# Kernel tuning notes

Hardware: AMD Instinct MI355X
Metric: run time of the kernel (lower is better)

The kernel has to match this reference:

```python
import jax, jax.numpy as jnp
import numpy as np

B, P1, P2 = 64, 15, 14            # batch, H/patch+1, W/patch
E0, E1, E2 = 8, 8, 8               # embed_dim per mode (512 total)
H1, H2, H3 = 2, 2, 2               # heads per mode (8 heads total)
X, Y, Z = E0 // H1, E1 // H2, E2 // H3  # per-head dims (4,4,4) -> head_dim 64
SCALE = (X * Y * Z) ** -0.5


def tle(x, W0, W1, W2, b):
    # mode-n products on last three modes (ignore_modes=(0,1,2)) + bias
    y = jnp.einsum('bpqxyz,ax->bpqayz', x, W0)
    y = jnp.einsum('bpqayz,cy->bpqacz', y, W1)
    y = jnp.einsum('bpqacz,dz->bpqacd', y, W2)
    return y + b


def split_heads(t):
    b, p, q = t.shape[:3]
    t = t.reshape(b, p, q, X, H1, Y, H2, Z, H3)
    return t.transpose(0, 1, 2, 4, 6, 8, 3, 5, 7)


def attention_core(x, Wq0, Wq1, Wq2, bq, Wk0, Wk1, Wk2, bk,
                   Wv0, Wv1, Wv2, bv, Wo0, Wo1, Wo2, bo):
    Q = split_heads(tle(x, Wq0, Wq1, Wq2, bq))
    K = split_heads(tle(x, Wk0, Wk1, Wk2, bk))
    V = split_heads(tle(x, Wv0, Wv1, Wv2, bv))
    # scores over spatial patch pairs per (h1,h2,h3) head triple
    attn = jnp.einsum('bpqdefxyz,bmndefxyz->bdefpqmn', Q, K) * SCALE
    b, d, e, f, p, q, m, n = attn.shape
    a = jax.nn.softmax(attn.reshape(b, d, e, f, p, q, m * n), axis=-1)
    a = a.reshape(b, d, e, f, p, q, m, n)
    o = jnp.einsum('bdefpqmn,bmndefxyz->bdefpqxyz', a, V)
    # b h1 h2 h3 p q x y z -> b p q (x h1)(y h2)(z h3)
    o = o.transpose(0, 4, 5, 6, 1, 7, 2, 8, 3).reshape(b, p, q, E0, E1, E2)
    return tle(o, Wo0, Wo1, Wo2, bo)


def setup_inputs() -> dict:
    key = jax.random.key(0)
    ks = jax.random.split(key, 17)
    inp = {'x': jax.random.normal(ks[0], (B, P1, P2, E0, E1, E2), jnp.float32)}
    i = 1
    for name in ('q', 'k', 'v', 'o'):
        for mode, dim in enumerate((E0, E1, E2)):
            inp[f'W{name}{mode}'] = jax.random.normal(ks[i], (dim, dim), jnp.float32) * 0.1
            i += 1
        inp[f'b{name}'] = jax.random.normal(ks[i], (E0, E1, E2), jnp.float32) * 0.02
        i += 1
    return inp


def reference(x, Wq0, Wq1, Wq2, bq, Wk0, Wk1, Wk2, bk,
              Wv0, Wv1, Wv2, bv, Wo0, Wo1, Wo2, bo):
    return attention_core(x, Wq0, Wq1, Wq2, bq, Wk0, Wk1, Wk2, bk,
                          Wv0, Wv1, Wv2, bv, Wo0, Wo1, Wo2, bo)
```

## Files before the change

### kernel.cpp

```cpp
#include <hip/hip_runtime.h>

typedef unsigned int   u32;
typedef unsigned short u16;
typedef float f32x16 __attribute__((ext_vector_type(16)));
typedef short s16x8  __attribute__((ext_vector_type(8)));
typedef u32   u32x4  __attribute__((ext_vector_type(4)));
typedef u32   u32x2  __attribute__((ext_vector_type(2)));

#define B_   64
#define P1_  15
#define P2_  14
#define S_   210
#define SP_  224
#define NT_  (B_*S_)
#define E_   512
#define NH_  8
#define HD_  64
#define KSC  0.18033688011112042f

__device__ __forceinline__ u16 f2bf(float f) {
    u32 u = __float_as_uint(f);
    u += 0x7fffu + ((u >> 16) & 1u);
    return (u16)(u >> 16);
}
__device__ __forceinline__ float bf2f(u16 h) {
    return __uint_as_float(((u32)h) << 16);
}

__device__ __forceinline__ void wfence() {
    asm volatile("s_waitcnt lgkmcnt(0)" ::: "memory");
}

__device__ __forceinline__ void mode_proj(
        const float* xs, float* t1, float* t2,
        const float* __restrict__ W0, const float* __restrict__ W1,
        const float* __restrict__ W2, const float* __restrict__ bb,
        int t, float* y3)
{
    {
        float xv[8];
        #pragma unroll
        for (int i = 0; i < 8; ++i) xv[i] = xs[i*66 + t];
        #pragma unroll
        for (int a = 0; a < 8; ++a) {
            float acc = 0.f;
            #pragma unroll
            for (int i = 0; i < 8; ++i) acc = fmaf(W0[a*8+i], xv[i], acc);
            t1[a*68 + t] = acc;
        }
    }
    wfence();
    {
        const int a = t >> 3, z = t & 7;
        float yv[8];
        #pragma unroll
        for (int y = 0; y < 8; ++y) yv[y] = t1[a*68 + y*8 + z];
        #pragma unroll
        for (int c = 0; c < 8; ++c) {
            float acc = 0.f;
            #pragma unroll
            for (int y = 0; y < 8; ++y) acc = fmaf(W1[c*8+y], yv[y], acc);
            t2[(a*8 + c)*9 + z] = acc;
        }
    }
    wfence();
    {
        float zv[8];
        #pragma unroll
        for (int z = 0; z < 8; ++z) zv[z] = t2[t*9 + z];
        #pragma unroll
        for (int d = 0; d < 8; ++d) {
            float acc = bb[t*8 + d];
            #pragma unroll
            for (int z = 0; z < 8; ++z) acc = fmaf(W2[d*8+z], zv[z], acc);
            y3[d] = acc;
        }
    }
    wfence();
}

__global__ __launch_bounds__(256) void k_qkv(
    const float* __restrict__ x,
    const float* __restrict__ Wq0, const float* __restrict__ Wq1,
    const float* __restrict__ Wq2, const float* __restrict__ bq,
    const float* __restrict__ Wk0, const float* __restrict__ Wk1,
    const float* __restrict__ Wk2, const float* __restrict__ bk,
    const float* __restrict__ Wv0, const float* __restrict__ Wv1,
    const float* __restrict__ Wv2, const float* __restrict__ bv,
    u16* __restrict__ Qo, u16* __restrict__ Ko, u16* __restrict__ Vo)
{
    __shared__ float xs[4][528];
    __shared__ float t1[4][544];
    __shared__ float t2[4][576];
    const int w = threadIdx.x >> 6, t = threadIdx.x & 63;
    const int tok = blockIdx.x*4 + w;
    const int b   = tok / S_;
    const int s   = tok - b * S_;

    const float* xp = x + (size_t)tok * E_;
    #pragma unroll
    for (int k4 = 0; k4 < 2; ++k4) {
        const float4 vv = *reinterpret_cast<const float4*>(xp + k4*256 + t*4);
        const int m0 = k4*4 + (t >> 4);
        const int in = (t*4) & 63;
        xs[w][m0*66 + in + 0] = vv.x;
        xs[w][m0*66 + in + 1] = vv.y;
        xs[w][m0*66 + in + 2] = vv.z;
        xs[w][m0*66 + in + 3] = vv.w;
    }
    wfence();

    const int a  = t >> 3, c = t & 7;
    const int x_ = a >> 1, h1 = a & 1;
    const int y_ = c >> 1, h2 = c & 1;

    float y3[8];

    mode_proj(xs[w], t1[w], t2[w], Wq0, Wq1, Wq2, bq, t, y3);
    #pragma unroll
    for (int h3 = 0; h3 < 2; ++h3) {
        const int h = (((h1 << 1) | h2) << 1) | h3;
        ushort4 v;
        v.x = f2bf(y3[0 + h3]); v.y = f2bf(y3[2 + h3]);
        v.z = f2bf(y3[4 + h3]); v.w = f2bf(y3[6 + h3]);
        *reinterpret_cast<ushort4*>(
            Qo + ((size_t)(b*NH_ + h)*SP_ + s)*HD_ + (x_*16 + y_*4)) = v;
    }
    mode_proj(xs[w], t1[w], t2[w], Wk0, Wk1, Wk2, bk, t, y3);
    #pragma unroll
    for (int h3 = 0; h3 < 2; ++h3) {
        const int h = (((h1 << 1) | h2) << 1) | h3;
        ushort4 v;
        v.x = f2bf(y3[0 + h3]); v.y = f2bf(y3[2 + h3]);
        v.z = f2bf(y3[4 + h3]); v.w = f2bf(y3[6 + h3]);
        *reinterpret_cast<ushort4*>(
            Ko + ((size_t)(b*NH_ + h)*SP_ + s)*HD_ + (x_*16 + y_*4)) = v;
    }
    mode_proj(xs[w], t1[w], t2[w], Wv0, Wv1, Wv2, bv, t, y3);
    #pragma unroll
    for (int h3 = 0; h3 < 2; ++h3) {
        const int h = (((h1 << 1) | h2) << 1) | h3;
        ushort4 v;
        v.x = f2bf(y3[0 + h3]); v.y = f2bf(y3[2 + h3]);
        v.z = f2bf(y3[4 + h3]); v.w = f2bf(y3[6 + h3]);
        *reinterpret_cast<ushort4*>(
            Vo + ((size_t)(b*NH_ + h)*SP_ + s)*HD_ + (x_*16 + y_*4)) = v;
    }
}

__global__ __launch_bounds__(512, 2) void k_attn(
    const u16* __restrict__ Q, const u16* __restrict__ K,
    const u16* __restrict__ V, u16* __restrict__ O)
{
    __shared__ u16   Kl[SP_*64];
    __shared__ u16   Vt[64*232];
    __shared__ float invl[8*32];

    const int bh  = blockIdx.x;
    const int tid = threadIdx.x;
    const u16* Qg = Q + (size_t)bh*SP_*HD_;
    const u16* Kg = K + (size_t)bh*SP_*HD_;
    const u16* Vg = V + (size_t)bh*SP_*HD_;

    #pragma unroll
    for (int i = 0; i < 4; ++i) {
        int sIdx = i*512 + tid;
        if (sIdx < 1792) {
            int row = sIdx >> 3, cc = sIdx & 7;
            u32x4 d = *(const u32x4*)(Kg + sIdx*8);
            *(u32x4*)&Kl[row*64 + (cc ^ (row & 7))*8] = d;
        }
    }
    if (tid < 448) {
        int tokg = tid >> 3, dg = tid & 7;
        int t0 = tokg*4, d0 = dg*8;
        u32x4 r0 = *(const u32x4*)(Vg + (size_t)(t0+0)*64 + d0);
        u32x4 r1 = *(const u32x4*)(Vg + (size_t)(t0+1)*64 + d0);
        u32x4 r2 = *(const u32x4*)(Vg + (size_t)(t0+2)*64 + d0);
        u32x4 r3 = *(const u32x4*)(Vg + (size_t)(t0+3)*64 + d0);
        #pragma unroll
        for (int j = 0; j < 8; ++j) {
            u32 sel = (j & 1) ? 0x07060302u : 0x05040100u;
            u32 lo  = __builtin_amdgcn_perm(r1[j>>1], r0[j>>1], sel);
            u32 hi2 = __builtin_amdgcn_perm(r3[j>>1], r2[j>>1], sel);
            *(u32x2*)&Vt[(d0+j)*232 + t0] = (u32x2){lo, hi2};
        }
    }
    __syncthreads();

    const int w    = tid >> 6;
    const int lane = tid & 63;
    const int l31  = lane & 31;
    const int hi   = lane >> 5;
    if (w >= 7) return;
    const int strip = w;

    const u16* qb = Qg + (size_t)(strip*32 + l31)*64 + hi*8;
    const s16x8 qf0 = *(const s16x8*)(qb +  0);
    const s16x8 qf1 = *(const s16x8*)(qb + 16);
    const s16x8 qf2 = *(const s16x8*)(qb + 32);
    const s16x8 qf3 = *(const s16x8*)(qb + 48);

    f32x16 oacc0 = {}, oacc1 = {};
    float  psum  = 0.f;
    const int swz = l31 & 7;

    #pragma unroll
    for (int kt = 0; kt < 7; ++kt) {
        const u16* kbase = &Kl[(kt*32 + l31)*64];
        f32x16 sacc = {};
        s16x8 kf;
        kf = *(const s16x8*)(kbase + ((0 + hi) ^ swz)*8);
        sacc = __builtin_amdgcn_mfma_f32_32x32x16_bf16(kf, qf0, sacc, 0, 0, 0);
        kf = *(const s16x8*)(kbase + ((2 + hi) ^ swz)*8);
        sacc = __builtin_amdgcn_mfma_f32_32x32x16_bf16(kf, qf1, sacc, 0, 0, 0);
        kf = *(const s16x8*)(kbase + ((4 + hi) ^ swz)*8);
        sacc = __builtin_amdgcn_mfma_f32_32x32x16_bf16(kf, qf2, sacc, 0, 0, 0);
        kf = *(const s16x8*)(kbase + ((6 + hi) ^ swz)*8);
        sacc = __builtin_amdgcn_mfma_f32_32x32x16_bf16(kf, qf3, sacc, 0, 0, 0);

        float p[16];
        #pragma unroll
        for (int r = 0; r < 16; ++r) p[r] = exp2f(sacc[r] * KSC);
        if (kt == 6) {
            const float hm = hi ? 0.f : 1.f;
            p[8] *= hm; p[9] *= hm;
            p[10] = 0.f; p[11] = 0.f; p[12] = 0.f; p[13] = 0.f; p[14] = 0.f; p[15] = 0.f;
        }
        #pragma unroll
        for (int r = 0; r < 16; ++r) psum += p[r];

        u32 c0, c1, c2, c3, c4, c5, c6, c7;
        asm("v_cvt_pk_bf16_f32 %0, %1, %2" : "=v"(c0) : "v"(p[0]),  "v"(p[1]));
        asm("v_cvt_pk_bf16_f32 %0, %1, %2" : "=v"(c1) : "v"(p[2]),  "v"(p[3]));
        asm("v_cvt_pk_bf16_f32 %0, %1, %2" : "=v"(c2) : "v"(p[4]),  "v"(p[5]));
        asm("v_cvt_pk_bf16_f32 %0, %1, %2" : "=v"(c3) : "v"(p[6]),  "v"(p[7]));
        asm("v_cvt_pk_bf16_f32 %0, %1, %2" : "=v"(c4) : "v"(p[8]),  "v"(p[9]));
        asm("v_cvt_pk_bf16_f32 %0, %1, %2" : "=v"(c5) : "v"(p[10]), "v"(p[11]));
        asm("v_cvt_pk_bf16_f32 %0, %1, %2" : "=v"(c6) : "v"(p[12]), "v"(p[13]));
        asm("v_cvt_pk_bf16_f32 %0, %1, %2" : "=v"(c7) : "v"(p[14]), "v"(p[15]));
        asm("v_permlane32_swap_b32 %0, %1" : "+v"(c0), "+v"(c2));
        asm("v_permlane32_swap_b32 %0, %1" : "+v"(c1), "+v"(c3));
        asm("v_permlane32_swap_b32 %0, %1" : "+v"(c4), "+v"(c6));
        asm("v_permlane32_swap_b32 %0, %1" : "+v"(c5), "+v"(c7));
        const s16x8 pf0 = __builtin_bit_cast(s16x8, (u32x4){c0, c1, c2, c3});
        const s16x8 pf1 = __builtin_bit_cast(s16x8, (u32x4){c4, c5, c6, c7});

        const u16* vb = &Vt[kt*32 + hi*8];
        s16x8 vf;
        vf = *(const s16x8*)(vb + (0*32 + l31)*232 +  0);
        oacc0 = __builtin_amdgcn_mfma_f32_32x32x16_bf16(pf0, vf, oacc0, 0, 0, 0);
        vf = *(const s16x8*)(vb + (0*32 + l31)*232 + 16);
        oacc0 = __builtin_amdgcn_mfma_f32_32x32x16_bf16(pf1, vf, oacc0, 0, 0, 0);
        vf = *(const s16x8*)(vb + (1*32 + l31)*232 +  0);
        oacc1 = __builtin_amdgcn_mfma_f32_32x32x16_bf16(pf0, vf, oacc1, 0, 0, 0);
        vf = *(const s16x8*)(vb + (1*32 + l31)*232 + 16);
        oacc1 = __builtin_amdgcn_mfma_f32_32x32x16_bf16(pf1, vf, oacc1, 0, 0, 0);
    }

    float tot = psum + __shfl_xor(psum, 32, 64);
    invl[w*32 + l31] = 1.0f / tot;
    asm volatile("s_waitcnt lgkmcnt(0)" ::: "memory");

    u16* Ob = O + ((size_t)bh*S_ + strip*32)*HD_;
    #pragma unroll
    for (int r = 0; r < 16; ++r) {
        const int q = (r & 3) + 8*(r >> 2) + 4*hi;
        if (strip == 6 && q >= 18) continue;
        const float iv = invl[w*32 + q];
        Ob[(size_t)q*64 + l31]      = f2bf(oacc0[r] * iv);
        Ob[(size_t)q*64 + 32 + l31] = f2bf(oacc1[r] * iv);
    }
}

__global__ __launch_bounds__(256) void k_oproj(
    const u16* __restrict__ O,
    const float* __restrict__ Wo0, const float* __restrict__ Wo1,
    const float* __restrict__ Wo2, const float* __restrict__ bo,
    float* __restrict__ out)
{
    __shared__ float xs[4][528];
    __shared__ float t1[4][544];
    __shared__ float t2[4][576];
    const int w = threadIdx.x >> 6, t = threadIdx.x & 63;
    const int tok = blockIdx.x*4 + w;
    const int b   = tok / S_;
    const int s   = tok - b * S_;

    const int a  = t >> 3, c = t & 7;
    const int x_ = a >> 1, h1 = a & 1;
    const int y_ = c >> 1, h2 = c & 1;
    #pragma unroll
    for (int h3 = 0; h3 < 2; ++h3) {
        const int h = (((h1 << 1) | h2) << 1) | h3;
        const ushort4 v = *reinterpret_cast<const ushort4*>(
            O + ((size_t)(b*NH_ + h)*S_ + s)*HD_ + (x_*16 + y_*4));
        xs[w][a*66 + c*8 + 0 + h3] = bf2f(v.x);
        xs[w][a*66 + c*8 + 2 + h3] = bf2f(v.y);
        xs[w][a*66 + c*8 + 4 + h3] = bf2f(v.z);
        xs[w][a*66 + c*8 + 6 + h3] = bf2f(v.w);
    }
    wfence();

    float y3[8];
    mode_proj(xs[w], t1[w], t2[w], Wo0, Wo1, Wo2, bo, t, y3);

    float4* op = reinterpret_cast<float4*>(out + (size_t)tok * E_ + t * 8);
    float4 u0, u1;
    u0.x = y3[0]; u0.y = y3[1]; u0.z = y3[2]; u0.w = y3[3];
    u1.x = y3[4]; u1.y = y3[5]; u1.z = y3[6]; u1.w = y3[7];
    op[0] = u0;
    op[1] = u1;
}

extern "C" void kernel_launch(void* const* d_in, const int* in_sizes, int n_in,
                              void* d_out, int out_size, void* d_ws, size_t ws_size,
                              hipStream_t stream)
{
    const float* x   = (const float*)d_in[0];
    const float* Wq0 = (const float*)d_in[1];
    const float* Wq1 = (const float*)d_in[2];
    const float* Wq2 = (const float*)d_in[3];
    const float* bq  = (const float*)d_in[4];
    const float* Wk0 = (const float*)d_in[5];
    const float* Wk1 = (const float*)d_in[6];
    const float* Wk2 = (const float*)d_in[7];
    const float* bk  = (const float*)d_in[8];
    const float* Wv0 = (const float*)d_in[9];
    const float* Wv1 = (const float*)d_in[10];
    const float* Wv2 = (const float*)d_in[11];
    const float* bv  = (const float*)d_in[12];
    const float* Wo0 = (const float*)d_in[13];
    const float* Wo1 = (const float*)d_in[14];
    const float* Wo2 = (const float*)d_in[15];
    const float* bo  = (const float*)d_in[16];

    const size_t TP = (size_t)B_ * NH_ * SP_ * HD_;
    u16* Qs = (u16*)d_ws;
    u16* Ks = Qs + TP;
    u16* Vs = Ks + TP;
    u16* Os = Vs + TP;

    k_qkv<<<NT_/4, 256, 0, stream>>>(x, Wq0, Wq1, Wq2, bq,
                                     Wk0, Wk1, Wk2, bk,
                                     Wv0, Wv1, Wv2, bv, Qs, Ks, Vs);
    k_attn<<<B_*NH_, 512, 0, stream>>>(Qs, Ks, Vs, Os);
    k_oproj<<<NT_/4, 256, 0, stream>>>(Os, Wo0, Wo1, Wo2, bo, (float*)d_out);
}
```

Measured before the change: 148.7 us.

## Prefetch Q before sync, batch LDS loads with MFMA priority, widen projection blocks

The attention kernel now issues its Q fragment loads before staging K/V and the barrier, so global latency overlaps the shared-memory fill. It groups the K and V fragment reads ahead of their MFMA chains and wraps the chains in s_setprio. The projection kernels handle 8 tokens per 512-thread block instead of 4, and QKV outputs use the packed v_cvt_pk_bf16_f32 conversion. Larger blocks raise LDS use per block, and the hardware conversion's rounding may differ slightly from the manual round-to-nearest-even.

Result: slower. 152.9 us (+2.8%).

```diff
diff --git a/kernel.cpp b/kernel.cpp
--- a/kernel.cpp
+++ b/kernel.cpp
@@ -26,6 +26,11 @@
 __device__ __forceinline__ float bf2f(u16 h) {
     return __uint_as_float(((u32)h) << 16);
 }
+__device__ __forceinline__ u32 cvtpk(float lo, float hi) {
+    u32 r;
+    asm("v_cvt_pk_bf16_f32 %0, %1, %2" : "=v"(r) : "v"(lo), "v"(hi));
+    return r;
+}
 
 __device__ __forceinline__ void wfence() {
     asm volatile("s_waitcnt lgkmcnt(0)" ::: "memory");
@@ -79,7 +84,7 @@
     wfence();
 }
 
-__global__ __launch_bounds__(256) void k_qkv(
+__global__ __launch_bounds__(512) void k_qkv(
     const float* __restrict__ x,
     const float* __restrict__ Wq0, const float* __restrict__ Wq1,
     const float* __restrict__ Wq2, const float* __restrict__ bq,
@@ -89,11 +94,11 @@
     const float* __restrict__ Wv2, const float* __restrict__ bv,
     u16* __restrict__ Qo, u16* __restrict__ Ko, u16* __restrict__ Vo)
 {
-    __shared__ float xs[4][528];
-    __shared__ float t1[4][544];
-    __shared__ float t2[4][576];
+    __shared__ float xs[8][528];
+    __shared__ float t1[8][544];
+    __shared__ float t2[8][576];
     const int w = threadIdx.x >> 6, t = threadIdx.x & 63;
-    const int tok = blockIdx.x*4 + w;
+    const int tok = blockIdx.x*8 + w;
     const int b   = tok / S_;
     const int s   = tok - b * S_;
 
@@ -120,31 +125,31 @@
     #pragma unroll
     for (int h3 = 0; h3 < 2; ++h3) {
         const int h = (((h1 << 1) | h2) << 1) | h3;
-        ushort4 v;
-        v.x = f2bf(y3[0 + h3]); v.y = f2bf(y3[2 + h3]);
-        v.z = f2bf(y3[4 + h3]); v.w = f2bf(y3[6 + h3]);
-        *reinterpret_cast<ushort4*>(
-            Qo + ((size_t)(b*NH_ + h)*SP_ + s)*HD_ + (x_*16 + y_*4)) = v;
+        u32x2 pk;
+        pk[0] = cvtpk(y3[0 + h3], y3[2 + h3]);
+        pk[1] = cvtpk(y3[4 + h3], y3[6 + h3]);
+        *reinterpret_cast<u32x2*>(
+            Qo + ((size_t)(b*NH_ + h)*SP_ + s)*HD_ + (x_*16 + y_*4)) = pk;
     }
     mode_proj(xs[w], t1[w], t2[w], Wk0, Wk1, Wk2, bk, t, y3);
     #pragma unroll
     for (int h3 = 0; h3 < 2; ++h3) {
         const int h = (((h1 << 1) | h2) << 1) | h3;
-        ushort4 v;
-        v.x = f2bf(y3[0 + h3]); v.y = f2bf(y3[2 + h3]);
-        v.z = f2bf(y3[4 + h3]); v.w = f2bf(y3[6 + h3]);
-        *reinterpret_cast<ushort4*>(
-            Ko + ((size_t)(b*NH_ + h)*SP_ + s)*HD_ + (x_*16 + y_*4)) = v;
+        u32x2 pk;
+        pk[0] = cvtpk(y3[0 + h3], y3[2 + h3]);
+        pk[1] = cvtpk(y3[4 + h3], y3[6 + h3]);
+        *reinterpret_cast<u32x2*>(
+            Ko + ((size_t)(b*NH_ + h)*SP_ + s)*HD_ + (x_*16 + y_*4)) = pk;
     }
     mode_proj(xs[w], t1[w], t2[w], Wv0, Wv1, Wv2, bv, t, y3);
     #pragma unroll
     for (int h3 = 0; h3 < 2; ++h3) {
         const int h = (((h1 << 1) | h2) << 1) | h3;
-        ushort4 v;
-        v.x = f2bf(y3[0 + h3]); v.y = f2bf(y3[2 + h3]);
-        v.z = f2bf(y3[4 + h3]); v.w = f2bf(y3[6 + h3]);
-        *reinterpret_cast<ushort4*>(
-            Vo + ((size_t)(b*NH_ + h)*SP_ + s)*HD_ + (x_*16 + y_*4)) = v;
+        u32x2 pk;
+        pk[0] = cvtpk(y3[0 + h3], y3[2 + h3]);
+        pk[1] = cvtpk(y3[4 + h3], y3[6 + h3]);
+        *reinterpret_cast<u32x2*>(
+            Vo + ((size_t)(b*NH_ + h)*SP_ + s)*HD_ + (x_*16 + y_*4)) = pk;
     }
 }
 
@@ -161,6 +166,18 @@
     const u16* Qg = Q + (size_t)bh*SP_*HD_;
     const u16* Kg = K + (size_t)bh*SP_*HD_;
     const u16* Vg = V + (size_t)bh*SP_*HD_;
+
+    const int w    = tid >> 6;
+    const int lane = tid & 63;
+    const int l31  = lane & 31;
+    const int hi   = lane >> 5;
+    const int strip = (w < 7) ? w : 6;
+
+    const u16* qb = Qg + (size_t)(strip*32 + l31)*64 + hi*8;
+    const s16x8 qf0 = *(const s16x8*)(qb +  0);
+    const s16x8 qf1 = *(const s16x8*)(qb + 16);
+    const s16x8 qf2 = *(const s16x8*)(qb + 32);
+    const s16x8 qf3 = *(const s16x8*)(qb + 48);
 
     #pragma unroll
     for (int i = 0; i < 4; ++i) {
@@ -188,18 +205,7 @@
     }
     __syncthreads();
 
-    const int w    = tid >> 6;
-    const int lane = tid & 63;
-    const int l31  = lane & 31;
-    const int hi   = lane >> 5;
     if (w >= 7) return;
-    const int strip = w;
-
-    const u16* qb = Qg + (size_t)(strip*32 + l31)*64 + hi*8;
-    const s16x8 qf0 = *(const s16x8*)(qb +  0);
-    const s16x8 qf1 = *(const s16x8*)(qb + 16);
-    const s16x8 qf2 = *(const s16x8*)(qb + 32);
-    const s16x8 qf3 = *(const s16x8*)(qb + 48);
 
     f32x16 oacc0 = {}, oacc1 = {};
     float  psum  = 0.f;
@@ -209,15 +215,16 @@
     for (int kt = 0; kt < 7; ++kt) {
         const u16* kbase = &Kl[(kt*32 + l31)*64];
         f32x16 sacc = {};
-        s16x8 kf;
-        kf = *(const s16x8*)(kbase + ((0 + hi) ^ swz)*8);
-        sacc = __builtin_amdgcn_mfma_f32_32x32x16_bf16(kf, qf0, sacc, 0, 0, 0);
-        kf = *(const s16x8*)(kbase + ((2 + hi) ^ swz)*8);
-        sacc = __builtin_amdgcn_mfma_f32_32x32x16_bf16(kf, qf1, sacc, 0, 0, 0);
-        kf = *(const s16x8*)(kbase + ((4 + hi) ^ swz)*8);
-        sacc = __builtin_amdgcn_mfma_f32_32x32x16_bf16(kf, qf2, sacc, 0, 0, 0);
-        kf = *(const s16x8*)(kbase + ((6 + hi) ^ swz)*8);
-        sacc = __builtin_amdgcn_mfma_f32_32x32x16_bf16(kf, qf3, sacc, 0, 0, 0);
+        s16x8 kf0 = *(const s16x8*)(kbase + ((0 + hi) ^ swz)*8);
+        s16x8 kf1 = *(const s16x8*)(kbase + ((2 + hi) ^ swz)*8);
+        s16x8 kf2 = *(const s16x8*)(kbase + ((4 + hi) ^ swz)*8);
+        s16x8 kf3 = *(const s16x8*)(kbase + ((6 + hi) ^ swz)*8);
+        __builtin_amdgcn_s_setprio(1);
+        sacc = __builtin_amdgcn_mfma_f32_32x32x16_bf16(kf0, qf0, sacc, 0, 0, 0);
+        sacc = __builtin_amdgcn_mfma_f32_32x32x16_bf16(kf1, qf1, sacc, 0, 0, 0);
+        sacc = __builtin_amdgcn_mfma_f32_32x32x16_bf16(kf2, qf2, sacc, 0, 0, 0);
+        sacc = __builtin_amdgcn_mfma_f32_32x32x16_bf16(kf3, qf3, sacc, 0, 0, 0);
+        __builtin_amdgcn_s_setprio(0);
 
         float p[16];
         #pragma unroll
@@ -247,15 +254,16 @@
         const s16x8 pf1 = __builtin_bit_cast(s16x8, (u32x4){c4, c5, c6, c7});
 
         const u16* vb = &Vt[kt*32 + hi*8];
-        s16x8 vf;
-        vf = *(const s16x8*)(vb + (0*32 + l31)*232 +  0);
-        oacc0 = __builtin_amdgcn_mfma_f32_32x32x16_bf16(pf0, vf, oacc0, 0, 0, 0);
-        vf = *(const s16x8*)(vb + (0*32 + l31)*232 + 16);
-        oacc0 = __builtin_amdgcn_mfma_f32_32x32x16_bf16(pf1, vf, oacc0, 0, 0, 0);
-        vf = *(const s16x8*)(vb + (1*32 + l31)*232 +  0);
-        oacc1 = __builtin_amdgcn_mfma_f32_32x32x16_bf16(pf0, vf, oacc1, 0, 0, 0);
-        vf = *(const s16x8*)(vb + (1*32 + l31)*232 + 16);
-        oacc1 = __builtin_amdgcn_mfma_f32_32x32x16_bf16(pf1, vf, oacc1, 0, 0, 0);
+        s16x8 vf0 = *(const s16x8*)(vb + (0*32 + l31)*232 +  0);
+        s16x8 vf1 = *(const s16x8*)(vb + (0*32 + l31)*232 + 16);
+        s16x8 vf2 = *(const s16x8*)(vb + (1*32 + l31)*232 +  0);
+        s16x8 vf3 = *(const s16x8*)(vb + (1*32 + l31)*232 + 16);
+        __builtin_amdgcn_s_setprio(1);
+        oacc0 = __builtin_amdgcn_mfma_f32_32x32x16_bf16(pf0, vf0, oacc0, 0, 0, 0);
+        oacc0 = __builtin_amdgcn_mfma_f32_32x32x16_bf16(pf1, vf1, oacc0, 0, 0, 0);
+        oacc1 = __builtin_amdgcn_mfma_f32_32x32x16_bf16(pf0, vf2, oacc1, 0, 0, 0);
+        oacc1 = __builtin_amdgcn_mfma_f32_32x32x16_bf16(pf1, vf3, oacc1, 0, 0, 0);
+        __builtin_amdgcn_s_setprio(0);
     }
 
     float tot = psum + __shfl_xor(psum, 32, 64);
@@ -273,17 +281,17 @@
     }
 }
 
-__global__ __launch_bounds__(256) void k_oproj(
+__global__ __launch_bounds__(512) void k_oproj(
     const u16* __restrict__ O,
     const float* __restrict__ Wo0, const float* __restrict__ Wo1,
     const float* __restrict__ Wo2, const float* __restrict__ bo,
     float* __restrict__ out)
 {
-    __shared__ float xs[4][528];
-    __shared__ float t1[4][544];
-    __shared__ float t2[4][576];
+    __shared__ float xs[8][528];
+    __shared__ float t1[8][544];
+    __shared__ float t2[8][576];
     const int w = threadIdx.x >> 6, t = threadIdx.x & 63;
-    const int tok = blockIdx.x*4 + w;
+    const int tok = blockIdx.x*8 + w;
     const int b   = tok / S_;
     const int s   = tok - b * S_;
 
@@ -341,9 +349,9 @@
     u16* Vs = Ks + TP;
     u16* Os = Vs + TP;
 
-    k_qkv<<<NT_/4, 256, 0, stream>>>(x, Wq0, Wq1, Wq2, bq,
+    k_qkv<<<NT_/8, 512, 0, stream>>>(x, Wq0, Wq1, Wq2, bq,
                                      Wk0, Wk1, Wk2, bk,
                                      Wv0, Wv1, Wv2, bv, Qs, Ks, Vs);
     k_attn<<<B_*NH_, 512, 0, stream>>>(Qs, Ks, Vs, Os);
-    k_oproj<<<NT_/4, 256, 0, stream>>>(Os, Wo0, Wo1, Wo2, bo, (float*)d_out);
-}
+    k_oproj<<<NT_/8, 512, 0, stream>>>(Os, Wo0, Wo1, Wo2, bo, (float*)d_out);
+}
```
